# Kernel tuning notes

Measured on AMD Instinct MI355X. Metric: run time of the kernel, lower is better.

## Reference

```python
import jax, jax.numpy as jnp
import numpy as np

CUTOFF = 5.0
LOG2 = float(np.log(2.0))

def ssp(x):
    # shifted softplus: softplus(x) - log(2)
    return jax.nn.softplus(x) - LOG2

def setup_inputs() -> dict:
    key = jax.random.key(0)
    ks = jax.random.split(key, 12)
    Nb, Na, Nnbh = 8, 1024, 64
    A, F, S = 128, 128, 50
    x = jax.random.normal(ks[0], (Nb, Na, A), dtype=jnp.float32)
    r_ij = jax.random.uniform(ks[1], (Nb, Na, Nnbh), dtype=jnp.float32) * 8.0  # some beyond cutoff=5
    neighbors = jax.random.randint(ks[2], (Nb, Na, Nnbh), 0, Na)
    neighbor_mask = (jax.random.uniform(ks[3], (Nb, Na, Nnbh)) > 0.1).astype(jnp.float32)
    f_ij = jax.random.normal(ks[4], (Nb, Na, Nnbh, S), dtype=jnp.float32)
    sc = lambda n: 1.0 / np.sqrt(n)
    W_in2f = jax.random.normal(ks[5], (F, A), dtype=jnp.float32) * sc(A)
    W_f1 = jax.random.normal(ks[6], (F, S), dtype=jnp.float32) * sc(S)
    b_f1 = jnp.zeros((F,), jnp.float32)
    W_f2 = jax.random.normal(ks[7], (F, F), dtype=jnp.float32) * sc(F)
    b_f2 = jnp.zeros((F,), jnp.float32)
    W_f2out = jax.random.normal(ks[8], (A, F), dtype=jnp.float32) * sc(F)
    b_f2out = jnp.zeros((A,), jnp.float32)
    W_dense = jax.random.normal(ks[9], (A, A), dtype=jnp.float32) * sc(A)
    b_dense = jnp.zeros((A,), jnp.float32)
    return {"x": x, "r_ij": r_ij, "neighbors": neighbors, "neighbor_mask": neighbor_mask,
            "f_ij": f_ij, "W_in2f": W_in2f, "W_f1": W_f1, "b_f1": b_f1, "W_f2": W_f2,
            "b_f2": b_f2, "W_f2out": W_f2out, "b_f2out": b_f2out, "W_dense": W_dense,
            "b_dense": b_dense}

def reference(x, r_ij, neighbors, neighbor_mask, f_ij, W_in2f, W_f1, b_f1, W_f2, b_f2,
              W_f2out, b_f2out, W_dense, b_dense):
    # filter network: Dense(S->F, ssp) -> Dense(F->F)
    W = ssp(jnp.einsum('bans,fs->banf', f_ij, W_f1) + b_f1)
    W = jnp.einsum('bang,fg->banf', W, W_f2) + b_f2          # [Nb,Na,Nnbh,F]
    # hard cutoff
    C = (r_ij <= CUTOFF).astype(W.dtype)                      # [Nb,Na,Nnbh]
    W = W * C[..., None]
    # in2f (no bias)
    y = jnp.einsum('bai,fi->baf', x, W_in2f)                  # [Nb,Na,F]
    # gather neighbor features along atom axis
    yg = jax.vmap(lambda yb, nb: yb[nb])(y, neighbors)        # [Nb,Na,Nnbh,F]
    # masked sum over neighbor axis (Aggregate, mean=False)
    v = jnp.sum(yg * W * neighbor_mask[..., None], axis=2)    # [Nb,Na,F]
    # f2out: Dense(F->A) with ssp, then dense: Dense(A->A)
    v = ssp(jnp.einsum('baf,af->ba' + 'f'[0:0] + 'a'[0:0], v, W_f2out).reshape(v.shape[:2] + (W_f2out.shape[0],)) if False else ssp(v @ W_f2out.T + b_f2out))
    out = v @ W_dense.T + b_dense                             # [Nb,Na,A]
    return out
```

## Files before the change

### kernel.cpp

```cpp
#include <hip/hip_runtime.h>
#include <math.h>


#define RCUT  5.0f
#define LOG2F_ 0.69314718055994530942f

typedef __bf16 bf16x8_t __attribute__((ext_vector_type(8)));
typedef float  f32x4_t  __attribute__((ext_vector_type(4)));

static __device__ __forceinline__ float sspf(float x) {
    return fmaxf(x, 0.0f) + __logf(1.0f + __expf(-fabsf(x))) - LOG2F_;
}
static __device__ __forceinline__ unsigned pack2h(__bf16 a, __bf16 b) {
    union { __bf16 h[2]; unsigned u; } un; un.h[0] = a; un.h[1] = b; return un.u;
}
static __device__ __forceinline__ unsigned pack2f(float a, float b) {
    return pack2h((__bf16)a, (__bf16)b);
}

__global__ __launch_bounds__(256, 4) void k1_prep_kernel(
    const float* __restrict__ x, const float* __restrict__ Wf,
    float* __restrict__ yout,
    const float* __restrict__ W1, const float* __restrict__ W2,
    const float* __restrict__ Wb,
    const float* __restrict__ Wc,
    unsigned* __restrict__ prep)
{
    __shared__ __bf16 Ah[16 * 136];
    __shared__ __bf16 Al[16 * 136];

    const int t = threadIdx.x;
    const int atom0 = blockIdx.x * 16;
    const int l = t & 63, m = l & 15, q = l >> 4;
    const int w = t >> 6;
    const int f0 = 32 * w + m;
    const int f1 = f0 + 16;

    {
        int i = blockIdx.x * 256 + t;
        if (i < 4096) {
            int sw = i >> 10, ft = (i >> 9) & 1, kh = (i >> 8) & 1;
            int sl = (i >> 2) & 63, j = i & 3;
            int sq = sl >> 4, sm = sl & 15;
            int f = 32 * sw + 16 * ft + sm;
            int c = kh * 16 + 4 * sq + j;
            int k0 = 2 * c, k1 = 2 * c + 1;
            float a = (k0 < 50) ? W1[f * 50 + k0] : 0.0f;
            float b = (k1 < 50) ? W1[f * 50 + k1] : 0.0f;
            prep[i] = pack2f(a, b);
        } else if (i < 12288) {
            int s = i - 4096;
            int sw = s >> 11, ft = (s >> 10) & 1, kq = (s >> 8) & 3;
            int sl = (s >> 2) & 63, j = s & 3;
            int sq = sl >> 4, sm = sl & 15;
            int f = 32 * sw + 16 * ft + sm;
            int c = 16 * kq + 4 * sq + j;
            float2 wv = ((const float2*)W2)[f * 64 + c];
            prep[i] = pack2f(wv.x, wv.y);
        } else if (i < 45056) {
            int s = i - 12288;
            int L = s >> 14;
            int r = s & 16383;
            int hl = r >> 13;
            int e = r & 8191;
            int sw = e >> 11, ft = (e >> 10) & 1, kq = (e >> 8) & 3;
            int sl = (e >> 2) & 63, j = e & 3;
            int sq = sl >> 4, sm = sl & 15;
            int f = 32 * sw + 16 * ft + sm;
            int c = 16 * kq + 4 * sq + j;
            const float* src = L ? Wc : Wb;
            float2 wv = ((const float2*)src)[f * 64 + c];
            if (hl == 0) {
                prep[i] = pack2h((__bf16)wv.x, (__bf16)wv.y);
            } else {
                __bf16 h0 = (__bf16)wv.x, h1 = (__bf16)wv.y;
                prep[i] = pack2f(wv.x - (float)h0, wv.y - (float)h1);
            }
        }
    }

    {
        const float4* A4 = (const float4*)(x + (size_t)atom0 * 128);
        unsigned* AhU = (unsigned*)Ah;
        unsigned* AlU = (unsigned*)Al;
        #pragma unroll
        for (int r = 0; r < 2; ++r) {
            int lin4 = r * 256 + t;
            int a = lin4 >> 5, k4 = lin4 & 31;
            float4 xv = A4[lin4];
            __bf16 h0=(__bf16)xv.x, h1=(__bf16)xv.y, h2=(__bf16)xv.z, h3=(__bf16)xv.w;
            int idx = a * 68 + 2 * k4;
            AhU[idx]     = pack2h(h0, h1);
            AhU[idx + 1] = pack2h(h2, h3);
            AlU[idx]     = pack2f(xv.x - (float)h0, xv.y - (float)h1);
            AlU[idx + 1] = pack2f(xv.z - (float)h2, xv.w - (float)h3);
        }
    }
    __syncthreads();

    f32x4_t acc0 = {0.f, 0.f, 0.f, 0.f};
    f32x4_t acc1 = {0.f, 0.f, 0.f, 0.f};
    #pragma unroll
    for (int kk = 0; kk < 4; ++kk) {
        bf16x8_t ah = *(const bf16x8_t*)&Ah[m * 136 + 32 * kk + 8 * q];
        bf16x8_t al = *(const bf16x8_t*)&Al[m * 136 + 32 * kk + 8 * q];
        #pragma unroll
        for (int ftl = 0; ftl < 2; ++ftl) {
            const float* wr = Wf + (size_t)(ftl ? f1 : f0) * 128 + 32 * kk + 8 * q;
            float4 wa = *(const float4*)wr;
            float4 wb4 = *(const float4*)(wr + 4);
            float wv[8] = {wa.x, wa.y, wa.z, wa.w, wb4.x, wb4.y, wb4.z, wb4.w};
            union { __bf16 h[8]; bf16x8_t v8; } wh, wl;
            #pragma unroll
            for (int k = 0; k < 8; ++k) {
                __bf16 hi = (__bf16)wv[k];
                wh.h[k] = hi;
                wl.h[k] = (__bf16)(wv[k] - (float)hi);
            }
            f32x4_t& acc = ftl ? acc1 : acc0;
            acc = __builtin_amdgcn_mfma_f32_16x16x32_bf16(ah, wh.v8, acc, 0, 0, 0);
            acc = __builtin_amdgcn_mfma_f32_16x16x32_bf16(ah, wl.v8, acc, 0, 0, 0);
            acc = __builtin_amdgcn_mfma_f32_16x16x32_bf16(al, wh.v8, acc, 0, 0, 0);
        }
    }
    #pragma unroll
    for (int r = 0; r < 4; ++r) {
        size_t row = (size_t)(atom0 + 4 * q + r) * 128;
        yout[row + f0] = acc0[r];
        yout[row + f1] = acc1[r];
    }
}

__global__ __launch_bounds__(256, 4) void interaction_kernel(
    const float* __restrict__ rij, const int* __restrict__ nbrs,
    const float* __restrict__ mask, const float* __restrict__ fij,
    const float* __restrict__ b1, const float* __restrict__ b2,
    const unsigned* __restrict__ W1S,
    const unsigned* __restrict__ W2S,
    const float* __restrict__ y, float* __restrict__ v)
{
    __shared__ __bf16 Hh[64 * 136];
    __shared__ __bf16 Hl[64 * 136];
    __shared__ float  cb[64];
    __shared__ int    nb[64];

    const int t  = threadIdx.x;
    const int a  = blockIdx.x;
    const int bi = a >> 10;
    const int p0 = a * 64;
    const int w = t >> 6, l = t & 63, m = l & 15, q = l >> 4;
    const int f0 = 32 * w + m;
    const int f1 = f0 + 16;

    if (t < 64) {
        float r = rij[p0 + t];
        cb[t] = (r <= RCUT) ? mask[p0 + t] : 0.0f;
        nb[t] = (bi << 10) + nbrs[p0 + t];
    }

    const float bb1_0 = b1[f0], bb1_1 = b1[f1];
    const float bb2_0 = b2[f0], bb2_1 = b2[f1];

    bf16x8_t w1f00 = *(const bf16x8_t*)(W1S + ((w * 2 + 0) * 2 + 0) * 256 + l * 4);
    bf16x8_t w1f01 = *(const bf16x8_t*)(W1S + ((w * 2 + 0) * 2 + 1) * 256 + l * 4);
    bf16x8_t w1f10 = *(const bf16x8_t*)(W1S + ((w * 2 + 1) * 2 + 0) * 256 + l * 4);
    bf16x8_t w1f11 = *(const bf16x8_t*)(W1S + ((w * 2 + 1) * 2 + 1) * 256 + l * 4);

    #pragma unroll 1
    for (int mt = 0; mt < 4; ++mt) {
        const float* frow = fij + (size_t)(p0 + 16 * mt + m) * 50;
        float kv[16];
        #pragma unroll
        for (int j2 = 0; j2 < 4; ++j2) {
            float2 xv = *(const float2*)(frow + 8 * q + 2 * j2);
            kv[2 * j2] = xv.x; kv[2 * j2 + 1] = xv.y;
        }
        #pragma unroll
        for (int j2 = 0; j2 < 4; ++j2) {
            int k = 32 + 8 * q + 2 * j2;
            float2 xv = make_float2(0.f, 0.f);
            if (k < 50) xv = *(const float2*)(frow + k);
            kv[8 + 2 * j2] = xv.x; kv[9 + 2 * j2] = xv.y;
        }
        union { __bf16 h[16]; bf16x8_t v8[2]; } uh, ul;
        #pragma unroll
        for (int k = 0; k < 16; ++k) {
            __bf16 hi = (__bf16)kv[k];
            uh.h[k] = hi;
            ul.h[k] = (__bf16)(kv[k] - (float)hi);
        }
        f32x4_t acc0 = {bb1_0, bb1_0, bb1_0, bb1_0};
        f32x4_t acc1 = {bb1_1, bb1_1, bb1_1, bb1_1};
        acc0 = __builtin_amdgcn_mfma_f32_16x16x32_bf16(uh.v8[0], w1f00, acc0, 0, 0, 0);
        acc0 = __builtin_amdgcn_mfma_f32_16x16x32_bf16(ul.v8[0], w1f00, acc0, 0, 0, 0);
        acc0 = __builtin_amdgcn_mfma_f32_16x16x32_bf16(uh.v8[1], w1f01, acc0, 0, 0, 0);
        acc0 = __builtin_amdgcn_mfma_f32_16x16x32_bf16(ul.v8[1], w1f01, acc0, 0, 0, 0);
        acc1 = __builtin_amdgcn_mfma_f32_16x16x32_bf16(uh.v8[0], w1f10, acc1, 0, 0, 0);
        acc1 = __builtin_amdgcn_mfma_f32_16x16x32_bf16(ul.v8[0], w1f10, acc1, 0, 0, 0);
        acc1 = __builtin_amdgcn_mfma_f32_16x16x32_bf16(uh.v8[1], w1f11, acc1, 0, 0, 0);
        acc1 = __builtin_amdgcn_mfma_f32_16x16x32_bf16(ul.v8[1], w1f11, acc1, 0, 0, 0);
        #pragma unroll
        for (int r = 0; r < 4; ++r) {
            int n = 16 * mt + 4 * q + r;
            float h0v = sspf(acc0[r]);
            float h1v = sspf(acc1[r]);
            __bf16 hh0 = (__bf16)h0v, hh1 = (__bf16)h1v;
            Hh[n * 136 + f0] = hh0;
            Hl[n * 136 + f0] = (__bf16)(h0v - (float)hh0);
            Hh[n * 136 + f1] = hh1;
            Hl[n * 136 + f1] = (__bf16)(h1v - (float)hh1);
        }
    }
    __syncthreads();

    float pv0 = 0.0f, pv1 = 0.0f;
    #pragma unroll 1
    for (int mt = 0; mt < 4; ++mt) {
        f32x4_t acc0 = {bb2_0, bb2_0, bb2_0, bb2_0};
        f32x4_t acc1 = {bb2_1, bb2_1, bb2_1, bb2_1};
        #pragma unroll
        for (int kq = 0; kq < 4; ++kq) {
            int hoff = (16 * mt + m) * 136 + 32 * kq + 8 * q;
            bf16x8_t hh = *(const bf16x8_t*)&Hh[hoff];
            bf16x8_t hl = *(const bf16x8_t*)&Hl[hoff];
            bf16x8_t w20 = *(const bf16x8_t*)(W2S + ((w * 2 + 0) * 4 + kq) * 256 + l * 4);
            bf16x8_t w21 = *(const bf16x8_t*)(W2S + ((w * 2 + 1) * 4 + kq) * 256 + l * 4);
            acc0 = __builtin_amdgcn_mfma_f32_16x16x32_bf16(hh, w20, acc0, 0, 0, 0);
            acc0 = __builtin_amdgcn_mfma_f32_16x16x32_bf16(hl, w20, acc0, 0, 0, 0);
            acc1 = __builtin_amdgcn_mfma_f32_16x16x32_bf16(hh, w21, acc1, 0, 0, 0);
            acc1 = __builtin_amdgcn_mfma_f32_16x16x32_bf16(hl, w21, acc1, 0, 0, 0);
        }
        #pragma unroll
        for (int r = 0; r < 4; ++r) {
            int n = 16 * mt + 4 * q + r;
            float cn = cb[n];
            const float* yrow = y + (size_t)nb[n] * 128;
            pv0 = fmaf(cn * yrow[f0], acc0[r], pv0);
            pv1 = fmaf(cn * yrow[f1], acc1[r], pv1);
        }
    }
    pv0 += __shfl_xor(pv0, 16);
    pv0 += __shfl_xor(pv0, 32);
    pv1 += __shfl_xor(pv1, 16);
    pv1 += __shfl_xor(pv1, 32);
    if (l < 16) {
        v[(size_t)a * 128 + f0] = pv0;
        v[(size_t)a * 128 + f1] = pv1;
    }
}

__global__ __launch_bounds__(256, 4) void mgemm2_kernel(
    const float* A,
    const unsigned* __restrict__ W1h, const unsigned* __restrict__ W1l,
    const float* __restrict__ bias1, int nssp1,
    const unsigned* __restrict__ W2h, const unsigned* __restrict__ W2l,
    const float* __restrict__ bias2, int nssp2,
    float* C)
{
    extern __shared__ float smf[];
    __bf16* Ah = (__bf16*)smf;
    __bf16* Al = (__bf16*)(smf + 1088);
    unsigned* AhU = (unsigned*)Ah;
    unsigned* AlU = (unsigned*)Al;

    const int t = threadIdx.x;
    const int atom0 = blockIdx.x * 16;
    const int w = t >> 6, l = t & 63, m = l & 15, q = l >> 4;

    {
        const float4* A4 = (const float4*)(A + (size_t)atom0 * 128);
        #pragma unroll
        for (int r = 0; r < 2; ++r) {
            int lin4 = r * 256 + t;
            int a = lin4 >> 5, k4 = lin4 & 31;
            float4 xv = A4[lin4];
            __bf16 h0=(__bf16)xv.x, h1=(__bf16)xv.y, h2=(__bf16)xv.z, h3=(__bf16)xv.w;
            int idx = a * 68 + 2 * k4;
            AhU[idx]     = pack2h(h0, h1);
            AhU[idx + 1] = pack2h(h2, h3);
            AlU[idx]     = pack2f(xv.x - (float)h0, xv.y - (float)h1);
            AlU[idx + 1] = pack2f(xv.z - (float)h2, xv.w - (float)h3);
        }
    }
    __syncthreads();

    bf16x8_t ah[4], al[4];
    #pragma unroll
    for (int kk = 0; kk < 4; ++kk) {
        int off = m * 136 + 32 * kk + 8 * q;
        ah[kk] = *(const bf16x8_t*)&Ah[off];
        al[kk] = *(const bf16x8_t*)&Al[off];
    }
    f32x4_t acc[2];
    int fidx[2];
    #pragma unroll
    for (int ft = 0; ft < 2; ++ft) {
        fidx[ft] = 16 * (2 * w + ft) + m;
        float b = bias1 ? bias1[fidx[ft]] : 0.0f;
        acc[ft] = (f32x4_t){b, b, b, b};
    }
    #pragma unroll
    for (int ft = 0; ft < 2; ++ft) {
        #pragma unroll
        for (int kk = 0; kk < 4; ++kk) {
            int wo = ((2 * w + ft) * 4 + kk) * 256 + l * 4;
            bf16x8_t wh = *(const bf16x8_t*)(W1h + wo);
            bf16x8_t wl = *(const bf16x8_t*)(W1l + wo);
            acc[ft] = __builtin_amdgcn_mfma_f32_16x16x32_bf16(ah[kk], wh, acc[ft], 0, 0, 0);
            acc[ft] = __builtin_amdgcn_mfma_f32_16x16x32_bf16(ah[kk], wl, acc[ft], 0, 0, 0);
            acc[ft] = __builtin_amdgcn_mfma_f32_16x16x32_bf16(al[kk], wh, acc[ft], 0, 0, 0);
        }
    }
    #pragma unroll
    for (int ft = 0; ft < 2; ++ft)
        #pragma unroll
        for (int r = 0; r < 4; ++r) {
            float o = acc[ft][r];
            if (nssp1 >= 1) o = sspf(o);
            if (nssp1 >= 2) o = sspf(o);
            acc[ft][r] = o;
        }

    __syncthreads();
    #pragma unroll
    for (int ft = 0; ft < 2; ++ft)
        #pragma unroll
        for (int r = 0; r < 4; ++r) {
            float o = acc[ft][r];
            __bf16 hh = (__bf16)o;
            Ah[(4 * q + r) * 136 + fidx[ft]] = hh;
            Al[(4 * q + r) * 136 + fidx[ft]] = (__bf16)(o - (float)hh);
        }
    __syncthreads();

    #pragma unroll
    for (int kk = 0; kk < 4; ++kk) {
        int off = m * 136 + 32 * kk + 8 * q;
        ah[kk] = *(const bf16x8_t*)&Ah[off];
        al[kk] = *(const bf16x8_t*)&Al[off];
    }
    #pragma unroll
    for (int ft = 0; ft < 2; ++ft) {
        float b = bias2 ? bias2[fidx[ft]] : 0.0f;
        acc[ft] = (f32x4_t){b, b, b, b};
    }
    #pragma unroll
    for (int ft = 0; ft < 2; ++ft) {
        #pragma unroll
        for (int kk = 0; kk < 4; ++kk) {
            int wo = ((2 * w + ft) * 4 + kk) * 256 + l * 4;
            bf16x8_t wh = *(const bf16x8_t*)(W2h + wo);
            bf16x8_t wl = *(const bf16x8_t*)(W2l + wo);
            acc[ft] = __builtin_amdgcn_mfma_f32_16x16x32_bf16(ah[kk], wh, acc[ft], 0, 0, 0);
            acc[ft] = __builtin_amdgcn_mfma_f32_16x16x32_bf16(ah[kk], wl, acc[ft], 0, 0, 0);
            acc[ft] = __builtin_amdgcn_mfma_f32_16x16x32_bf16(al[kk], wh, acc[ft], 0, 0, 0);
        }
    }
    #pragma unroll
    for (int ft = 0; ft < 2; ++ft)
        #pragma unroll
        for (int r = 0; r < 4; ++r) {
            float o = acc[ft][r];
            if (nssp2 >= 1) o = sspf(o);
            if (nssp2 >= 2) o = sspf(o);
            C[(size_t)(atom0 + 4 * q + r) * 128 + fidx[ft]] = o;
        }
}

extern "C" void kernel_launch(void* const* d_in, const int* in_sizes, int n_in,
                              void* d_out, int out_size, void* d_ws, size_t ws_size,
                              hipStream_t stream) {
    const float* x        = (const float*)d_in[0];
    const float* rij      = (const float*)d_in[1];
    const int*   nbrs     = (const int*)  d_in[2];
    const float* mask     = (const float*)d_in[3];
    const float* fij      = (const float*)d_in[4];
    const float* W_in2f   = (const float*)d_in[5];
    const float* W_f1     = (const float*)d_in[6];
    const float* b_f1     = (const float*)d_in[7];
    const float* W_f2     = (const float*)d_in[8];
    const float* b_f2     = (const float*)d_in[9];
    const float* W_f2out  = (const float*)d_in[10];
    const float* b_f2out  = (const float*)d_in[11];
    const float* W_dense  = (const float*)d_in[12];
    const float* b_dense  = (const float*)d_in[13];
    float* out = (float*)d_out;

    float*    y    = (float*)d_ws;
    unsigned* prep = (unsigned*)((char*)d_ws + (4u << 20));
    const unsigned* W1S   = prep;
    const unsigned* W2S   = prep + 4096;
    const unsigned* f2o_h = prep + 12288, *f2o_l = prep + 20480;
    const unsigned* den_h = prep + 28672, *den_l = prep + 36864;

    const int MG2_LDS = 2176 * 4;

    k1_prep_kernel<<<512, 256, 0, stream>>>(
        x, W_in2f, y, W_f1, W_f2, W_f2out, W_dense, prep);
    interaction_kernel<<<8192, 256, 0, stream>>>(
        rij, nbrs, mask, fij, b_f1, b_f2, W1S, W2S, y, out);
    mgemm2_kernel<<<512, 256, MG2_LDS, stream>>>(
        out, f2o_h, f2o_l, b_f2out, 2, den_h, den_l, b_dense, 0, out);
}
```

Baseline: 262.0 us.

## Split weight prep from in2f GEMM and restructure filter-network tiling

Moves the in2f weight split (bf16 hi/lo) into a separate prep kernel so the in2f GEMM kernel reads pre-split fragments and uses twice as many blocks, each computing one 16-column tile per wave. In the interaction kernel, the first filter layer now gives each wave one 16-row neighbor tile and loops over all 8 feature tiles, instead of each wave looping over 4 row tiles. W2 fragments are hoisted into registers before the second GEMM loop. Shifted softplus is rewritten with exp2/log2. This adds an extra kernel launch and more register pressure from the hoisted W2 fragments.

New measurement: 256.0 us. 2.3% less time.

```diff
diff --git a/kernel.cpp b/kernel.cpp
--- a/kernel.cpp
+++ b/kernel.cpp
@@ -4,12 +4,15 @@
 
 #define RCUT  5.0f
 #define LOG2F_ 0.69314718055994530942f
+#define LOG2E_ 1.44269504088896340736f
 
 typedef __bf16 bf16x8_t __attribute__((ext_vector_type(8)));
 typedef float  f32x4_t  __attribute__((ext_vector_type(4)));
 
 static __device__ __forceinline__ float sspf(float x) {
-    return fmaxf(x, 0.0f) + __logf(1.0f + __expf(-fabsf(x))) - LOG2F_;
+    float e  = exp2f(-LOG2E_ * fabsf(x));
+    float lg = log2f(1.0f + e);
+    return fmaf(lg, LOG2F_, fmaxf(x, 0.0f) - LOG2F_);
 }
 static __device__ __forceinline__ unsigned pack2h(__bf16 a, __bf16 b) {
     union { __bf16 h[2]; unsigned u; } un; un.h[0] = a; un.h[1] = b; return un.u;
@@ -18,66 +21,67 @@
     return pack2h((__bf16)a, (__bf16)b);
 }
 
-__global__ __launch_bounds__(256, 4) void k1_prep_kernel(
-    const float* __restrict__ x, const float* __restrict__ Wf,
-    float* __restrict__ yout,
+__global__ __launch_bounds__(256) void prep_kernel(
     const float* __restrict__ W1, const float* __restrict__ W2,
     const float* __restrict__ Wb,
     const float* __restrict__ Wc,
+    const float* __restrict__ Wf,
     unsigned* __restrict__ prep)
+{
+    int i = blockIdx.x * 256 + threadIdx.x;
+    if (i < 4096) {
+        int sw = i >> 10, ft = (i >> 9) & 1, kh = (i >> 8) & 1;
+        int sl = (i >> 2) & 63, j = i & 3;
+        int sq = sl >> 4, sm = sl & 15;
+        int f = 32 * sw + 16 * ft + sm;
+        int c = kh * 16 + 4 * sq + j;
+        int k0 = 2 * c, k1 = 2 * c + 1;
+        float a = (k0 < 50) ? W1[f * 50 + k0] : 0.0f;
+        float b = (k1 < 50) ? W1[f * 50 + k1] : 0.0f;
+        prep[i] = pack2f(a, b);
+    } else if (i < 12288) {
+        int s = i - 4096;
+        int sw = s >> 11, ft = (s >> 10) & 1, kq = (s >> 8) & 3;
+        int sl = (s >> 2) & 63, j = s & 3;
+        int sq = sl >> 4, sm = sl & 15;
+        int f = 32 * sw + 16 * ft + sm;
+        int c = 16 * kq + 4 * sq + j;
+        float2 wv = ((const float2*)W2)[f * 64 + c];
+        prep[i] = pack2f(wv.x, wv.y);
+    } else {
+        int s = i - 12288;
+        int L = s >> 14;
+        int r = s & 16383;
+        int hl = r >> 13;
+        int e = r & 8191;
+        int sw = e >> 11, ft = (e >> 10) & 1, kq = (e >> 8) & 3;
+        int sl = (e >> 2) & 63, j = e & 3;
+        int sq = sl >> 4, sm = sl & 15;
+        int f = 32 * sw + 16 * ft + sm;
+        int c = 16 * kq + 4 * sq + j;
+        const float* src = (L == 0) ? Wb : (L == 1) ? Wc : Wf;
+        float2 wv = ((const float2*)src)[f * 64 + c];
+        if (hl == 0) {
+            prep[i] = pack2h((__bf16)wv.x, (__bf16)wv.y);
+        } else {
+            __bf16 h0 = (__bf16)wv.x, h1 = (__bf16)wv.y;
+            prep[i] = pack2f(wv.x - (float)h0, wv.y - (float)h1);
+        }
+    }
+}
+
+__global__ __launch_bounds__(256, 4) void k1_kernel(
+    const float* __restrict__ x,
+    const unsigned* __restrict__ Wh, const unsigned* __restrict__ Wl,
+    float* __restrict__ yout)
 {
     __shared__ __bf16 Ah[16 * 136];
     __shared__ __bf16 Al[16 * 136];
 
     const int t = threadIdx.x;
-    const int atom0 = blockIdx.x * 16;
-    const int l = t & 63, m = l & 15, q = l >> 4;
-    const int w = t >> 6;
-    const int f0 = 32 * w + m;
-    const int f1 = f0 + 16;
-
-    {
-        int i = blockIdx.x * 256 + t;
-        if (i < 4096) {
-            int sw = i >> 10, ft = (i >> 9) & 1, kh = (i >> 8) & 1;
-            int sl = (i >> 2) & 63, j = i & 3;
-            int sq = sl >> 4, sm = sl & 15;
-            int f = 32 * sw + 16 * ft + sm;
-            int c = kh * 16 + 4 * sq + j;
-            int k0 = 2 * c, k1 = 2 * c + 1;
-            float a = (k0 < 50) ? W1[f * 50 + k0] : 0.0f;
-            float b = (k1 < 50) ? W1[f * 50 + k1] : 0.0f;
-            prep[i] = pack2f(a, b);
-        } else if (i < 12288) {
-            int s = i - 4096;
-            int sw = s >> 11, ft = (s >> 10) & 1, kq = (s >> 8) & 3;
-            int sl = (s >> 2) & 63, j = s & 3;
-            int sq = sl >> 4, sm = sl & 15;
-            int f = 32 * sw + 16 * ft + sm;
-            int c = 16 * kq + 4 * sq + j;
-            float2 wv = ((const float2*)W2)[f * 64 + c];
-            prep[i] = pack2f(wv.x, wv.y);
-        } else if (i < 45056) {
-            int s = i - 12288;
-            int L = s >> 14;
-            int r = s & 16383;
-            int hl = r >> 13;
-            int e = r & 8191;
-            int sw = e >> 11, ft = (e >> 10) & 1, kq = (e >> 8) & 3;
-            int sl = (e >> 2) & 63, j = e & 3;
-            int sq = sl >> 4, sm = sl & 15;
-            int f = 32 * sw + 16 * ft + sm;
-            int c = 16 * kq + 4 * sq + j;
-            const float* src = L ? Wc : Wb;
-            float2 wv = ((const float2*)src)[f * 64 + c];
-            if (hl == 0) {
-                prep[i] = pack2h((__bf16)wv.x, (__bf16)wv.y);
-            } else {
-                __bf16 h0 = (__bf16)wv.x, h1 = (__bf16)wv.y;
-                prep[i] = pack2f(wv.x - (float)h0, wv.y - (float)h1);
-            }
-        }
-    }
+    const int atom0 = (blockIdx.x >> 1) * 16;
+    const int fh = blockIdx.x & 1;
+    const int w = t >> 6, l = t & 63, m = l & 15, q = l >> 4;
 
     {
         const float4* A4 = (const float4*)(x + (size_t)atom0 * 128);
@@ -98,37 +102,24 @@
     }
     __syncthreads();
 
-    f32x4_t acc0 = {0.f, 0.f, 0.f, 0.f};
-    f32x4_t acc1 = {0.f, 0.f, 0.f, 0.f};
+    const int ftile = fh * 4 + w;
+    const int f = 16 * ftile + m;
+    f32x4_t acc = {0.f, 0.f, 0.f, 0.f};
     #pragma unroll
     for (int kk = 0; kk < 4; ++kk) {
-        bf16x8_t ah = *(const bf16x8_t*)&Ah[m * 136 + 32 * kk + 8 * q];
-        bf16x8_t al = *(const bf16x8_t*)&Al[m * 136 + 32 * kk + 8 * q];
-        #pragma unroll
-        for (int ftl = 0; ftl < 2; ++ftl) {
-            const float* wr = Wf + (size_t)(ftl ? f1 : f0) * 128 + 32 * kk + 8 * q;
-            float4 wa = *(const float4*)wr;
-            float4 wb4 = *(const float4*)(wr + 4);
-            float wv[8] = {wa.x, wa.y, wa.z, wa.w, wb4.x, wb4.y, wb4.z, wb4.w};
-            union { __bf16 h[8]; bf16x8_t v8; } wh, wl;
-            #pragma unroll
-            for (int k = 0; k < 8; ++k) {
-                __bf16 hi = (__bf16)wv[k];
-                wh.h[k] = hi;
-                wl.h[k] = (__bf16)(wv[k] - (float)hi);
-            }
-            f32x4_t& acc = ftl ? acc1 : acc0;
-            acc = __builtin_amdgcn_mfma_f32_16x16x32_bf16(ah, wh.v8, acc, 0, 0, 0);
-            acc = __builtin_amdgcn_mfma_f32_16x16x32_bf16(ah, wl.v8, acc, 0, 0, 0);
-            acc = __builtin_amdgcn_mfma_f32_16x16x32_bf16(al, wh.v8, acc, 0, 0, 0);
-        }
-    }
-    #pragma unroll
-    for (int r = 0; r < 4; ++r) {
-        size_t row = (size_t)(atom0 + 4 * q + r) * 128;
-        yout[row + f0] = acc0[r];
-        yout[row + f1] = acc1[r];
-    }
+        int off = m * 136 + 32 * kk + 8 * q;
+        bf16x8_t ah = *(const bf16x8_t*)&Ah[off];
+        bf16x8_t al = *(const bf16x8_t*)&Al[off];
+        int wo = (ftile * 4 + kk) * 256 + l * 4;
+        bf16x8_t wh = *(const bf16x8_t*)(Wh + wo);
+        bf16x8_t wl = *(const bf16x8_t*)(Wl + wo);
+        acc = __builtin_amdgcn_mfma_f32_16x16x32_bf16(ah, wh, acc, 0, 0, 0);
+        acc = __builtin_amdgcn_mfma_f32_16x16x32_bf16(ah, wl, acc, 0, 0, 0);
+        acc = __builtin_amdgcn_mfma_f32_16x16x32_bf16(al, wh, acc, 0, 0, 0);
+    }
+    #pragma unroll
+    for (int r = 0; r < 4; ++r)
+        yout[(size_t)(atom0 + 4 * q + r) * 128 + f] = acc[r];
 }
 
 __global__ __launch_bounds__(256, 4) void interaction_kernel(
@@ -149,8 +140,6 @@
     const int bi = a >> 10;
     const int p0 = a * 64;
     const int w = t >> 6, l = t & 63, m = l & 15, q = l >> 4;
-    const int f0 = 32 * w + m;
-    const int f1 = f0 + 16;
 
     if (t < 64) {
         float r = rij[p0 + t];
@@ -158,17 +147,8 @@
         nb[t] = (bi << 10) + nbrs[p0 + t];
     }
 
-    const float bb1_0 = b1[f0], bb1_1 = b1[f1];
-    const float bb2_0 = b2[f0], bb2_1 = b2[f1];
-
-    bf16x8_t w1f00 = *(const bf16x8_t*)(W1S + ((w * 2 + 0) * 2 + 0) * 256 + l * 4);
-    bf16x8_t w1f01 = *(const bf16x8_t*)(W1S + ((w * 2 + 0) * 2 + 1) * 256 + l * 4);
-    bf16x8_t w1f10 = *(const bf16x8_t*)(W1S + ((w * 2 + 1) * 2 + 0) * 256 + l * 4);
-    bf16x8_t w1f11 = *(const bf16x8_t*)(W1S + ((w * 2 + 1) * 2 + 1) * 256 + l * 4);
-
-    #pragma unroll 1
-    for (int mt = 0; mt < 4; ++mt) {
-        const float* frow = fij + (size_t)(p0 + 16 * mt + m) * 50;
+    {
+        const float* frow = fij + (size_t)(p0 + 16 * w + m) * 50;
         float kv[16];
         #pragma unroll
         for (int j2 = 0; j2 < 4; ++j2) {
@@ -189,30 +169,37 @@
             uh.h[k] = hi;
             ul.h[k] = (__bf16)(kv[k] - (float)hi);
         }
-        f32x4_t acc0 = {bb1_0, bb1_0, bb1_0, bb1_0};
-        f32x4_t acc1 = {bb1_1, bb1_1, bb1_1, bb1_1};
-        acc0 = __builtin_amdgcn_mfma_f32_16x16x32_bf16(uh.v8[0], w1f00, acc0, 0, 0, 0);
-        acc0 = __builtin_amdgcn_mfma_f32_16x16x32_bf16(ul.v8[0], w1f00, acc0, 0, 0, 0);
-        acc0 = __builtin_amdgcn_mfma_f32_16x16x32_bf16(uh.v8[1], w1f01, acc0, 0, 0, 0);
-        acc0 = __builtin_amdgcn_mfma_f32_16x16x32_bf16(ul.v8[1], w1f01, acc0, 0, 0, 0);
-        acc1 = __builtin_amdgcn_mfma_f32_16x16x32_bf16(uh.v8[0], w1f10, acc1, 0, 0, 0);
-        acc1 = __builtin_amdgcn_mfma_f32_16x16x32_bf16(ul.v8[0], w1f10, acc1, 0, 0, 0);
-        acc1 = __builtin_amdgcn_mfma_f32_16x16x32_bf16(uh.v8[1], w1f11, acc1, 0, 0, 0);
-        acc1 = __builtin_amdgcn_mfma_f32_16x16x32_bf16(ul.v8[1], w1f11, acc1, 0, 0, 0);
-        #pragma unroll
-        for (int r = 0; r < 4; ++r) {
-            int n = 16 * mt + 4 * q + r;
-            float h0v = sspf(acc0[r]);
-            float h1v = sspf(acc1[r]);
-            __bf16 hh0 = (__bf16)h0v, hh1 = (__bf16)h1v;
-            Hh[n * 136 + f0] = hh0;
-            Hl[n * 136 + f0] = (__bf16)(h0v - (float)hh0);
-            Hh[n * 136 + f1] = hh1;
-            Hl[n * 136 + f1] = (__bf16)(h1v - (float)hh1);
-        }
-    }
-    __syncthreads();
-
+        #pragma unroll 2
+        for (int ftile = 0; ftile < 8; ++ftile) {
+            float bb = b1[16 * ftile + m];
+            f32x4_t acc = {bb, bb, bb, bb};
+            bf16x8_t w0 = *(const bf16x8_t*)(W1S + (ftile * 2 + 0) * 256 + l * 4);
+            bf16x8_t w1 = *(const bf16x8_t*)(W1S + (ftile * 2 + 1) * 256 + l * 4);
+            acc = __builtin_amdgcn_mfma_f32_16x16x32_bf16(uh.v8[0], w0, acc, 0, 0, 0);
+            acc = __builtin_amdgcn_mfma_f32_16x16x32_bf16(ul.v8[0], w0, acc, 0, 0, 0);
+            acc = __builtin_amdgcn_mfma_f32_16x16x32_bf16(uh.v8[1], w1, acc, 0, 0, 0);
+            acc = __builtin_amdgcn_mfma_f32_16x16x32_bf16(ul.v8[1], w1, acc, 0, 0, 0);
+            #pragma unroll
+            for (int r = 0; r < 4; ++r) {
+                int n = 16 * w + 4 * q + r;
+                float hv = sspf(acc[r]);
+                __bf16 hh = (__bf16)hv;
+                Hh[n * 136 + 16 * ftile + m] = hh;
+                Hl[n * 136 + 16 * ftile + m] = (__bf16)(hv - (float)hh);
+            }
+        }
+    }
+    __syncthreads();
+
+    const int f0 = 32 * w + m;
+    const int f1 = f0 + 16;
+    const float bb2_0 = b2[f0], bb2_1 = b2[f1];
+    bf16x8_t w2f0[4], w2f1[4];
+    #pragma unroll
+    for (int kq = 0; kq < 4; ++kq) {
+        w2f0[kq] = *(const bf16x8_t*)(W2S + ((w * 2 + 0) * 4 + kq) * 256 + l * 4);
+        w2f1[kq] = *(const bf16x8_t*)(W2S + ((w * 2 + 1) * 4 + kq) * 256 + l * 4);
+    }
     float pv0 = 0.0f, pv1 = 0.0f;
     #pragma unroll 1
     for (int mt = 0; mt < 4; ++mt) {
@@ -223,12 +210,10 @@
             int hoff = (16 * mt + m) * 136 + 32 * kq + 8 * q;
             bf16x8_t hh = *(const bf16x8_t*)&Hh[hoff];
             bf16x8_t hl = *(const bf16x8_t*)&Hl[hoff];
-            bf16x8_t w20 = *(const bf16x8_t*)(W2S + ((w * 2 + 0) * 4 + kq) * 256 + l * 4);
-            bf16x8_t w21 = *(const bf16x8_t*)(W2S + ((w * 2 + 1) * 4 + kq) * 256 + l * 4);
-            acc0 = __builtin_amdgcn_mfma_f32_16x16x32_bf16(hh, w20, acc0, 0, 0, 0);
-            acc0 = __builtin_amdgcn_mfma_f32_16x16x32_bf16(hl, w20, acc0, 0, 0, 0);
-            acc1 = __builtin_amdgcn_mfma_f32_16x16x32_bf16(hh, w21, acc1, 0, 0, 0);
-            acc1 = __builtin_amdgcn_mfma_f32_16x16x32_bf16(hl, w21, acc1, 0, 0, 0);
+            acc0 = __builtin_amdgcn_mfma_f32_16x16x32_bf16(hh, w2f0[kq], acc0, 0, 0, 0);
+            acc0 = __builtin_amdgcn_mfma_f32_16x16x32_bf16(hl, w2f0[kq], acc0, 0, 0, 0);
+            acc1 = __builtin_amdgcn_mfma_f32_16x16x32_bf16(hh, w2f1[kq], acc1, 0, 0, 0);
+            acc1 = __builtin_amdgcn_mfma_f32_16x16x32_bf16(hl, w2f1[kq], acc1, 0, 0, 0);
         }
         #pragma unroll
         for (int r = 0; r < 4; ++r) {
@@ -388,15 +373,16 @@
 
     float*    y    = (float*)d_ws;
     unsigned* prep = (unsigned*)((char*)d_ws + (4u << 20));
-    const unsigned* W1S   = prep;
-    const unsigned* W2S   = prep + 4096;
-    const unsigned* f2o_h = prep + 12288, *f2o_l = prep + 20480;
-    const unsigned* den_h = prep + 28672, *den_l = prep + 36864;
+    const unsigned* W1S    = prep;
+    const unsigned* W2S    = prep + 4096;
+    const unsigned* f2o_h  = prep + 12288, *f2o_l  = prep + 20480;
+    const unsigned* den_h  = prep + 28672, *den_l  = prep + 36864;
+    const unsigned* in2f_h = prep + 45056, *in2f_l = prep + 53248;
 
     const int MG2_LDS = 2176 * 4;
 
-    k1_prep_kernel<<<512, 256, 0, stream>>>(
-        x, W_in2f, y, W_f1, W_f2, W_f2out, W_dense, prep);
+    prep_kernel<<<240, 256, 0, stream>>>(W_f1, W_f2, W_f2out, W_dense, W_in2f, prep);
+    k1_kernel<<<1024, 256, 0, stream>>>(x, in2f_h, in2f_l, y);
     interaction_kernel<<<8192, 256, 0, stream>>>(
         rij, nbrs, mask, fij, b_f1, b_f2, W1S, W2S, y, out);
     mgemm2_kernel<<<512, 256, MG2_LDS, stream>>>(
```
